# Performance work log

Hardware: AMD Instinct MI355X
Metric: run time of the kernel (lower is better)

The kernel has to match this reference:

```python
import jax, jax.numpy as jnp
import numpy as np

N, F_IN, F_OUT = 8192, 512, 256
NEG_BIG = -9e15


def setup_inputs() -> dict:
    key = jax.random.key(0)
    k1, k2, k3, k4, k5 = jax.random.split(key, 5)
    h = jax.random.normal(k1, (N, F_IN), dtype=jnp.float32)
    adj = jax.random.randint(k2, (N, N), 0, 2, dtype=jnp.int32)
    W = jax.random.normal(k3, (F_IN, F_OUT), dtype=jnp.float32) / np.sqrt(F_IN)
    bW = jnp.zeros((F_OUT,), dtype=jnp.float32)
    a1 = jax.random.normal(k4, (F_OUT,), dtype=jnp.float32) / np.sqrt(2 * F_OUT)
    a2 = jax.random.normal(k5, (F_OUT,), dtype=jnp.float32) / np.sqrt(2 * F_OUT)
    ba = jnp.zeros((), dtype=jnp.float32)
    return {"h": h, "adj": adj, "W": W, "bW": bW, "a1": a1, "a2": a2, "ba": ba}


def reference(h, adj, W, bW, a1, a2, ba):
    # Wh: [N, F_OUT]
    Wh = h @ W + bW
    # a([Wh_i ; Wh_j]) + b == (Wh_i . a1) + (Wh_j . a2) + b  (rank-1 decomposition,
    # avoids the O(N^2 * 2F) repeat/cat tensor the torch code materializes)
    f1 = Wh @ a1  # [N]
    f2 = Wh @ a2  # [N]
    e = jax.nn.leaky_relu(f1[:, None] + f2[None, :] + ba, negative_slope=0.2)
    e = jnp.where(adj > 0, e, NEG_BIG)
    attention = jax.nn.softmax(e, axis=1)  # dropout = identity (eval mode)
    return attention @ Wh
```

## Files before the change

kernel.cpp:

```cpp
#include <hip/hip_runtime.h>

typedef __bf16 bf16;
typedef __attribute__((ext_vector_type(4))) float f32x4;
typedef __attribute__((ext_vector_type(8))) __bf16 bf16x8;
typedef __attribute__((ext_vector_type(4))) __bf16 bf16x4;
typedef __attribute__((ext_vector_type(4))) int i32x4;

#define NN 8192
#define FI 512
#define FO 256
#define NSPLIT 4
#define JCHUNK (NN / NSPLIT)

__global__ __launch_bounds__(256) void k0_pack(const int* __restrict__ adj,
                                               unsigned* __restrict__ mask) {
  const int gid = blockIdx.x * 256 + threadIdx.x;
  const int* p = adj + (size_t)gid * 32;
  unsigned m = 0;
#pragma unroll
  for (int u = 0; u < 8; ++u) {
    i32x4 v = *(const i32x4*)(p + u * 4);
    m |= (unsigned)(v.x > 0) << (u * 4 + 0);
    m |= (unsigned)(v.y > 0) << (u * 4 + 1);
    m |= (unsigned)(v.z > 0) << (u * 4 + 2);
    m |= (unsigned)(v.w > 0) << (u * 4 + 3);
  }
  mask[gid] = m;
}

__global__ __launch_bounds__(256) void kw_split(const float* __restrict__ W,
                                                bf16* __restrict__ wth,
                                                bf16* __restrict__ wtl) {
  const int idx = blockIdx.x * 256 + threadIdx.x;
  const int k = idx >> 8, n = idx & 255;
  float x = W[idx];
  bf16 hi = (bf16)x;
  wth[(size_t)n * FI + k] = hi;
  wtl[(size_t)n * FI + k] = (bf16)(x - (float)hi);
}

__global__ __launch_bounds__(256) void k1_gemm(
    const float* __restrict__ h, const bf16* __restrict__ wth,
    const bf16* __restrict__ wtl, const float* __restrict__ bW,
    const float* __restrict__ a1, const float* __restrict__ a2,
    bf16* __restrict__ whb, float* __restrict__ f1, float* __restrict__ f2) {
  __shared__ bf16 Ah[32 * 40];
  __shared__ bf16 Al[32 * 40];
  const int t = threadIdx.x;
  const int lane = t & 63, w = t >> 6;
  const int m16 = lane & 15, q = lane >> 4;
  const int bi = blockIdx.x, bj = blockIdx.y;
  const int i0 = bi * 32;
  const int n0 = bj * 128 + w * 32;
  const int srow = t >> 3, skoff = (t & 7) * 4;

  const f32x4 z4 = {0.f, 0.f, 0.f, 0.f};
  f32x4 acc[2][2];
#pragma unroll
  for (int mt = 0; mt < 2; ++mt)
#pragma unroll
    for (int nt = 0; nt < 2; ++nt) acc[mt][nt] = z4;

  const float* hrow = h + (size_t)(i0 + srow) * FI + skoff;

  for (int kt = 0; kt < FI / 32; ++kt) {
    f32x4 hv = *(const f32x4*)(hrow + kt * 32);
    bf16x8 bh[2], bl[2];
#pragma unroll
    for (int nt = 0; nt < 2; ++nt) {
      const size_t woff = (size_t)(n0 + nt * 16 + m16) * FI + kt * 32 + q * 8;
      bh[nt] = *(const bf16x8*)(wth + woff);
      bl[nt] = *(const bf16x8*)(wtl + woff);
    }
    bf16x4 hh, hl;
#pragma unroll
    for (int x = 0; x < 4; ++x) {
      float v = hv[x];
      bf16 hi = (bf16)v;
      hh[x] = hi;
      hl[x] = (bf16)(v - (float)hi);
    }
    __syncthreads();
    *(bf16x4*)&Ah[srow * 40 + skoff] = hh;
    *(bf16x4*)&Al[srow * 40 + skoff] = hl;
    __syncthreads();
#pragma unroll
    for (int mt = 0; mt < 2; ++mt) {
      bf16x8 ah = *(const bf16x8*)&Ah[(mt * 16 + m16) * 40 + q * 8];
      bf16x8 al = *(const bf16x8*)&Al[(mt * 16 + m16) * 40 + q * 8];
#pragma unroll
      for (int nt = 0; nt < 2; ++nt) {
        acc[mt][nt] = __builtin_amdgcn_mfma_f32_16x16x32_bf16(ah, bh[nt], acc[mt][nt], 0, 0, 0);
        acc[mt][nt] = __builtin_amdgcn_mfma_f32_16x16x32_bf16(al, bh[nt], acc[mt][nt], 0, 0, 0);
        acc[mt][nt] = __builtin_amdgcn_mfma_f32_16x16x32_bf16(ah, bl[nt], acc[mt][nt], 0, 0, 0);
      }
    }
  }
  float f1p[2][4] = {}, f2p[2][4] = {};
#pragma unroll
  for (int nt = 0; nt < 2; ++nt) {
    const int n = n0 + nt * 16 + m16;
    const float bw = bW[n], av1 = a1[n], av2 = a2[n];
#pragma unroll
    for (int mt = 0; mt < 2; ++mt) {
#pragma unroll
      for (int reg = 0; reg < 4; ++reg) {
        float wh = acc[mt][nt][reg] + bw;
        const int il = mt * 16 + q * 4 + reg;
        whb[(size_t)bi * (FO * 32) + n * 32 + il] = (bf16)wh;
        f1p[mt][reg] += wh * av1;
        f2p[mt][reg] += wh * av2;
      }
    }
  }
#pragma unroll
  for (int m = 1; m < 16; m <<= 1) {
#pragma unroll
    for (int mt = 0; mt < 2; ++mt)
#pragma unroll
      for (int reg = 0; reg < 4; ++reg) {
        f1p[mt][reg] += __shfl_xor(f1p[mt][reg], m);
        f2p[mt][reg] += __shfl_xor(f2p[mt][reg], m);
      }
  }
  if (m16 == 0) {
#pragma unroll
    for (int mt = 0; mt < 2; ++mt)
#pragma unroll
      for (int reg = 0; reg < 4; ++reg) {
        const int i = i0 + mt * 16 + q * 4 + reg;
        atomicAdd(&f1[i], f1p[mt][reg]);
        atomicAdd(&f2[i], f2p[mt][reg]);
      }
  }
}

__global__ __launch_bounds__(256) void k3_max(const float* __restrict__ f2,
                                              float* __restrict__ Mstar) {
  __shared__ float red[4];
  const int t = threadIdx.x;
  float m = -1e30f;
  for (int i = t; i < NN; i += 256) m = fmaxf(m, f2[i]);
#pragma unroll
  for (int d = 1; d < 64; d <<= 1) m = fmaxf(m, __shfl_xor(m, d));
  if ((t & 63) == 0) red[t >> 6] = m;
  __syncthreads();
  if (t == 0) *Mstar = fmaxf(fmaxf(red[0], red[1]), fmaxf(red[2], red[3]));
}

__global__ __launch_bounds__(256) void k4_attn(
    const unsigned* __restrict__ mask, const bf16* __restrict__ whb,
    const float* __restrict__ f1, const float* __restrict__ f2,
    const float* __restrict__ Mstar, const float* __restrict__ ba_p,
    float* __restrict__ acc_part, float* __restrict__ l_part) {
  __shared__ bf16 Pl[64 * 40];
  const int t = threadIdx.x;
  const int lane = t & 63, w = t >> 6;
  const int m16 = lane & 15, q = lane >> 4;
  const int rb = blockIdx.x, s = blockIdx.y;
  const int i0 = rb * 64;
  const int rloc = t >> 2;
  const int jj = (t & 3) * 8;

  const float ba = *ba_p;
  const float Ms = *Mstar;
  const float ci = f1[i0 + rloc] + ba;
  float sh = ci + Ms;
  sh = fmaxf(sh, 0.2f * sh);

  const f32x4 z4 = {0.f, 0.f, 0.f, 0.f};
  f32x4 acc[4][4];
#pragma unroll
  for (int mt = 0; mt < 4; ++mt)
#pragma unroll
    for (int cc = 0; cc < 4; ++cc) acc[mt][cc] = z4;
  float lreg = 0.f;

  const unsigned* mrow = mask + (size_t)(i0 + rloc) * (NN / 32);
  const int sbase = s * JCHUNK;

  for (int kt = 0; kt < JCHUNK / 32; ++kt) {
    const int j0 = sbase + kt * 32;
    const unsigned mw = mrow[j0 >> 5];
    f32x4 s4a = *(const f32x4*)(f2 + j0 + jj);
    f32x4 s4b = *(const f32x4*)(f2 + j0 + jj + 4);
    const size_t bbase = (size_t)(j0 >> 5) * (FO * 32) + q * 8;
    bf16x8 bfr[4];
#pragma unroll
    for (int cc = 0; cc < 4; ++cc)
      bfr[cc] = *(const bf16x8*)(whb + bbase + (size_t)((w * 4 + cc) * 16 + m16) * 32);
    float pv[8];
#pragma unroll
    for (int x = 0; x < 4; ++x) {
      float arg = ci + s4a[x];
      float e = fmaxf(arg, 0.2f * arg);
      pv[x] = ((mw >> (jj + x)) & 1u) ? __expf(e - sh) : 0.f;
    }
#pragma unroll
    for (int x = 0; x < 4; ++x) {
      float arg = ci + s4b[x];
      float e = fmaxf(arg, 0.2f * arg);
      pv[4 + x] = ((mw >> (jj + 4 + x)) & 1u) ? __expf(e - sh) : 0.f;
    }
#pragma unroll
    for (int x = 0; x < 8; ++x) lreg += pv[x];
    __syncthreads();
    bf16x8 pb;
#pragma unroll
    for (int x = 0; x < 8; ++x) pb[x] = (bf16)pv[x];
    *(bf16x8*)&Pl[rloc * 40 + jj] = pb;
    __syncthreads();
#pragma unroll
    for (int mt = 0; mt < 4; ++mt) {
      bf16x8 af = *(const bf16x8*)&Pl[(mt * 16 + m16) * 40 + q * 8];
#pragma unroll
      for (int cc = 0; cc < 4; ++cc)
        acc[mt][cc] = __builtin_amdgcn_mfma_f32_16x16x32_bf16(af, bfr[cc], acc[mt][cc], 0, 0, 0);
    }
  }
  lreg += __shfl_xor(lreg, 1);
  lreg += __shfl_xor(lreg, 2);
  if ((t & 3) == 0) l_part[(size_t)s * NN + i0 + rloc] = lreg;
  float* ap = acc_part + (size_t)s * ((size_t)NN * FO);
#pragma unroll
  for (int mt = 0; mt < 4; ++mt) {
#pragma unroll
    for (int cc = 0; cc < 4; ++cc) {
      const int n = (w * 4 + cc) * 16 + m16;
#pragma unroll
      for (int reg = 0; reg < 4; ++reg) {
        const int r = i0 + mt * 16 + q * 4 + reg;
        ap[(size_t)r * FO + n] = acc[mt][cc][reg];
      }
    }
  }
}

__global__ __launch_bounds__(256) void k5_reduce(
    const float* __restrict__ accp, const float* __restrict__ lp,
    float* __restrict__ out) {
  const int idx = blockIdx.x * 256 + threadIdx.x;
  const int i = idx >> 6, n4 = (idx & 63) * 4;
  f32x4 sum = {0.f, 0.f, 0.f, 0.f};
  float l = 0.f;
#pragma unroll
  for (int s = 0; s < NSPLIT; ++s) {
    sum += *(const f32x4*)&accp[(size_t)s * ((size_t)NN * FO) + (size_t)i * FO + n4];
    l += lp[s * NN + i];
  }
  const float rl = 1.0f / l;
  f32x4 o = sum * rl;
  *(f32x4*)&out[(size_t)i * FO + n4] = o;
}

extern "C" void kernel_launch(void* const* d_in, const int* in_sizes, int n_in,
                              void* d_out, int out_size, void* d_ws, size_t ws_size,
                              hipStream_t stream) {
  const float* h   = (const float*)d_in[0];
  const int*   adj = (const int*)d_in[1];
  const float* W   = (const float*)d_in[2];
  const float* bW  = (const float*)d_in[3];
  const float* a1  = (const float*)d_in[4];
  const float* a2  = (const float*)d_in[5];
  const float* ba  = (const float*)d_in[6];
  float* out = (float*)d_out;

  char* ws = (char*)d_ws;
  bf16* whb   = (bf16*)ws;
  float* f1   = (float*)(ws + 4u * 1024 * 1024);
  float* f2   = (float*)(ws + 4u * 1024 * 1024 + 32 * 1024);
  float* Mst  = (float*)(ws + 4u * 1024 * 1024 + 64 * 1024);
  float* accp = (float*)(ws + 4u * 1024 * 1024 + 64 * 1024 + 256);
  float* lp   = accp + (size_t)NSPLIT * NN * FO;
  unsigned* mask = (unsigned*)((char*)lp + (size_t)NSPLIT * NN * 4);
  bf16* wth   = (bf16*)((char*)mask + (size_t)NN * (NN / 32) * 4);
  bf16* wtl   = wth + (size_t)FO * FI;

  hipMemsetAsync(f1, 0, 64 * 1024, stream);

  k0_pack<<<NN * (NN / 32) / 256, 256, 0, stream>>>(adj, mask);
  kw_split<<<FI * FO / 256, 256, 0, stream>>>(W, wth, wtl);
  k1_gemm<<<dim3(NN / 32, 2), 256, 0, stream>>>(h, wth, wtl, bW, a1, a2, whb, f1, f2);
  k3_max<<<1, 256, 0, stream>>>(f2, Mst);
  k4_attn<<<dim3(NN / 64, NSPLIT), 256, 0, stream>>>(mask, whb, f1, f2, Mst, ba, accp, lp);
  k5_reduce<<<(NN * FO / 4) / 256, 256, 0, stream>>>(accp, lp, out);
}
```

Baseline: 481.4 us.

## Fuse adjacency packing into attention kernel with register prefetch and more splits

Removes the separate bit-mask packing kernel; the attention kernel now reads the int32 adjacency directly and tests each entry. Loads of the adjacency, f2 and Wh fragments for the next step are issued before the LDS barrier, overlapping global latency with the MFMA work. NSPLIT is doubled to give more blocks. The cost is that each attention block reads 32x more adjacency bytes than the packed mask, and the workspace holds larger partial accumulators that the reduction must sum.

```diff
diff --git a/kernel.cpp b/kernel.cpp
--- a/kernel.cpp
+++ b/kernel.cpp
@@ -9,24 +9,9 @@
 #define NN 8192
 #define FI 512
 #define FO 256
-#define NSPLIT 4
+#define NSPLIT 8
 #define JCHUNK (NN / NSPLIT)
-
-__global__ __launch_bounds__(256) void k0_pack(const int* __restrict__ adj,
-                                               unsigned* __restrict__ mask) {
-  const int gid = blockIdx.x * 256 + threadIdx.x;
-  const int* p = adj + (size_t)gid * 32;
-  unsigned m = 0;
-#pragma unroll
-  for (int u = 0; u < 8; ++u) {
-    i32x4 v = *(const i32x4*)(p + u * 4);
-    m |= (unsigned)(v.x > 0) << (u * 4 + 0);
-    m |= (unsigned)(v.y > 0) << (u * 4 + 1);
-    m |= (unsigned)(v.z > 0) << (u * 4 + 2);
-    m |= (unsigned)(v.w > 0) << (u * 4 + 3);
-  }
-  mask[gid] = m;
-}
+#define KSTEPS (JCHUNK / 32)
 
 __global__ __launch_bounds__(256) void kw_split(const float* __restrict__ W,
                                                 bf16* __restrict__ wth,
@@ -149,7 +134,7 @@
 }
 
 __global__ __launch_bounds__(256) void k4_attn(
-    const unsigned* __restrict__ mask, const bf16* __restrict__ whb,
+    const int* __restrict__ adj, const bf16* __restrict__ whb,
     const float* __restrict__ f1, const float* __restrict__ f2,
     const float* __restrict__ Mstar, const float* __restrict__ ba_p,
     float* __restrict__ acc_part, float* __restrict__ l_part) {
@@ -176,40 +161,57 @@
     for (int cc = 0; cc < 4; ++cc) acc[mt][cc] = z4;
   float lreg = 0.f;
 
-  const unsigned* mrow = mask + (size_t)(i0 + rloc) * (NN / 32);
+  const int* arow = adj + (size_t)(i0 + rloc) * NN;
   const int sbase = s * JCHUNK;
 
-  for (int kt = 0; kt < JCHUNK / 32; ++kt) {
-    const int j0 = sbase + kt * 32;
-    const unsigned mw = mrow[j0 >> 5];
-    f32x4 s4a = *(const f32x4*)(f2 + j0 + jj);
-    f32x4 s4b = *(const f32x4*)(f2 + j0 + jj + 4);
-    const size_t bbase = (size_t)(j0 >> 5) * (FO * 32) + q * 8;
-    bf16x8 bfr[4];
+  i32x4 a4a = *(const i32x4*)(arow + sbase + jj);
+  i32x4 a4b = *(const i32x4*)(arow + sbase + jj + 4);
+  f32x4 s4a = *(const f32x4*)(f2 + sbase + jj);
+  f32x4 s4b = *(const f32x4*)(f2 + sbase + jj + 4);
+  bf16x8 bfr[4];
+  {
+    const size_t bbase = (size_t)(sbase >> 5) * (FO * 32) + q * 8;
 #pragma unroll
     for (int cc = 0; cc < 4; ++cc)
       bfr[cc] = *(const bf16x8*)(whb + bbase + (size_t)((w * 4 + cc) * 16 + m16) * 32);
+  }
+
+  for (int kt = 0; kt < KSTEPS; ++kt) {
     float pv[8];
 #pragma unroll
     for (int x = 0; x < 4; ++x) {
       float arg = ci + s4a[x];
       float e = fmaxf(arg, 0.2f * arg);
-      pv[x] = ((mw >> (jj + x)) & 1u) ? __expf(e - sh) : 0.f;
+      pv[x] = (a4a[x] > 0) ? __expf(e - sh) : 0.f;
     }
 #pragma unroll
     for (int x = 0; x < 4; ++x) {
       float arg = ci + s4b[x];
       float e = fmaxf(arg, 0.2f * arg);
-      pv[4 + x] = ((mw >> (jj + 4 + x)) & 1u) ? __expf(e - sh) : 0.f;
+      pv[4 + x] = (a4b[x] > 0) ? __expf(e - sh) : 0.f;
     }
 #pragma unroll
     for (int x = 0; x < 8; ++x) lreg += pv[x];
-    __syncthreads();
     bf16x8 pb;
 #pragma unroll
     for (int x = 0; x < 8; ++x) pb[x] = (bf16)pv[x];
+
+    const int ktn = (kt + 1 < KSTEPS) ? kt + 1 : kt;
+    const int j0n = sbase + ktn * 32;
+    i32x4 a4a_n = *(const i32x4*)(arow + j0n + jj);
+    i32x4 a4b_n = *(const i32x4*)(arow + j0n + jj + 4);
+    f32x4 s4a_n = *(const f32x4*)(f2 + j0n + jj);
+    f32x4 s4b_n = *(const f32x4*)(f2 + j0n + jj + 4);
+    bf16x8 bfn[4];
+    const size_t bbn = (size_t)(j0n >> 5) * (FO * 32) + q * 8;
+#pragma unroll
+    for (int cc = 0; cc < 4; ++cc)
+      bfn[cc] = *(const bf16x8*)(whb + bbn + (size_t)((w * 4 + cc) * 16 + m16) * 32);
+
+    __syncthreads();
     *(bf16x8*)&Pl[rloc * 40 + jj] = pb;
     __syncthreads();
+
 #pragma unroll
     for (int mt = 0; mt < 4; ++mt) {
       bf16x8 af = *(const bf16x8*)&Pl[(mt * 16 + m16) * 40 + q * 8];
@@ -217,6 +219,9 @@
       for (int cc = 0; cc < 4; ++cc)
         acc[mt][cc] = __builtin_amdgcn_mfma_f32_16x16x32_bf16(af, bfr[cc], acc[mt][cc], 0, 0, 0);
     }
+    a4a = a4a_n; a4b = a4b_n; s4a = s4a_n; s4b = s4b_n;
+#pragma unroll
+    for (int cc = 0; cc < 4; ++cc) bfr[cc] = bfn[cc];
   }
   lreg += __shfl_xor(lreg, 1);
   lreg += __shfl_xor(lreg, 2);
@@ -272,16 +277,14 @@
   float* Mst  = (float*)(ws + 4u * 1024 * 1024 + 64 * 1024);
   float* accp = (float*)(ws + 4u * 1024 * 1024 + 64 * 1024 + 256);
   float* lp   = accp + (size_t)NSPLIT * NN * FO;
-  unsigned* mask = (unsigned*)((char*)lp + (size_t)NSPLIT * NN * 4);
-  bf16* wth   = (bf16*)((char*)mask + (size_t)NN * (NN / 32) * 4);
+  bf16* wth   = (bf16*)((char*)lp + (size_t)NSPLIT * NN * 4);
   bf16* wtl   = wth + (size_t)FO * FI;
 
   hipMemsetAsync(f1, 0, 64 * 1024, stream);
 
-  k0_pack<<<NN * (NN / 32) / 256, 256, 0, stream>>>(adj, mask);
   kw_split<<<FI * FO / 256, 256, 0, stream>>>(W, wth, wtl);
   k1_gemm<<<dim3(NN / 32, 2), 256, 0, stream>>>(h, wth, wtl, bW, a1, a2, whb, f1, f2);
   k3_max<<<1, 256, 0, stream>>>(f2, Mst);
-  k4_attn<<<dim3(NN / 64, NSPLIT), 256, 0, stream>>>(mask, whb, f1, f2, Mst, ba, accp, lp);
+  k4_attn<<<dim3(NN / 64, NSPLIT), 256, 0, stream>>>(adj, whb, f1, f2, Mst, ba, accp, lp);
   k5_reduce<<<(NN * FO / 4) / 256, 256, 0, stream>>>(accp, lp, out);
 }
```

New measurement: 490.2 us. About the same (+1.8%).
